# Kernel optimization log

Measured on AMD Instinct MI355X. Metric: run time of the kernel, lower is better.

The kernel has to match this reference:

```python
import jax, jax.numpy as jnp
import numpy as np

N_NODES = 100_000
N_RAND_EDGES = 3_200_000
IN_FEATS, HIDDEN, N_CLASSES = 256, 32, 40


def setup_inputs() -> dict:
    key = jax.random.key(0)
    kf, ks, kd, kw1, kw2 = jax.random.split(key, 5)
    features = jax.random.normal(kf, (N_NODES, IN_FEATS), dtype=jnp.float32)
    # random edges + explicit self loops (mirrors dgl.add_self_loop)
    src = jnp.concatenate([
        jax.random.randint(ks, (N_RAND_EDGES,), 0, N_NODES, dtype=jnp.int32),
        jnp.arange(N_NODES, dtype=jnp.int32),
    ])
    dst = jnp.concatenate([
        jax.random.randint(kd, (N_RAND_EDGES,), 0, N_NODES, dtype=jnp.int32),
        jnp.arange(N_NODES, dtype=jnp.int32),
    ])
    # Glorot-style init as in DGL GraphConv
    W1 = jax.random.normal(kw1, (IN_FEATS, HIDDEN), dtype=jnp.float32) * (2.0 / (IN_FEATS + HIDDEN)) ** 0.5
    b1 = jnp.zeros((HIDDEN,), dtype=jnp.float32)
    W2 = jax.random.normal(kw2, (HIDDEN, N_CLASSES), dtype=jnp.float32) * (2.0 / (HIDDEN + N_CLASSES)) ** 0.5
    b2 = jnp.zeros((N_CLASSES,), dtype=jnp.float32)
    return {"features": features, "src": src, "dst": dst,
            "W1": W1, "b1": b1, "W2": W2, "b2": b2}


def _graph_conv(x, W, b, src, dst, norm_src, norm_dst):
    """DGL GraphConv, norm='both': D_in^{-1/2} A D_out^{-1/2} X W + b.
    Apply W first (cheaper gather when out_feats small); math-identical."""
    h = (x * norm_src[:, None]) @ W              # [N, out]
    msgs = h[src]                                # gather  [E, out]
    agg = jax.ops.segment_sum(msgs, dst, num_segments=N_NODES)  # scatter-add
    return agg * norm_dst[:, None] + b


def reference(features, src, dst, W1, b1, W2, b2):
    ones = jnp.ones(src.shape[0], dtype=jnp.float32)
    out_deg = jax.ops.segment_sum(ones, src, num_segments=N_NODES)
    in_deg = jax.ops.segment_sum(ones, dst, num_segments=N_NODES)
    norm_src = jax.lax.rsqrt(out_deg)            # self loops guarantee deg >= 1
    norm_dst = jax.lax.rsqrt(in_deg)

    x = _graph_conv(features, W1, b1, src, dst, norm_src, norm_dst)
    x = jax.nn.relu(x)
    # F.dropout(training=self.training) is identity at inference
    x = _graph_conv(x, W2, b2, src, dst, norm_src, norm_dst)
    return jax.nn.log_softmax(x, axis=1)
```

## Files before the change

### kernel.cpp

```cpp
#include <hip/hip_runtime.h>
#include <hip/hip_bf16.h>
#include <math.h>

#define BSHIFT 7
#define NBUCK(N) (((N) + 127) >> 7)
#define TILE 8192
#define CAP 5632

typedef short bf16x8 __attribute__((ext_vector_type(8)));
typedef float f32x16 __attribute__((ext_vector_type(16)));

__device__ __forceinline__ unsigned short f2bf(float f) {
    unsigned u = __float_as_uint(f);
    u += 0x7fffu + ((u >> 16) & 1u);
    return (unsigned short)(u >> 16);
}
__device__ __forceinline__ unsigned packbf2(float lo, float hi) {
    return (unsigned)f2bf(lo) | ((unsigned)f2bf(hi) << 16);
}
__device__ __forceinline__ float bf_lo(unsigned u) { return __uint_as_float(u << 16); }
__device__ __forceinline__ float bf_hi(unsigned u) { return __uint_as_float(u & 0xffff0000u); }

__global__ __launch_bounds__(256) void pg_kernel(
    const int* __restrict__ src, const int* __restrict__ dst,
    int* __restrict__ gcurD, int* __restrict__ gcurS,
    int* __restrict__ gbufD, unsigned char* __restrict__ gbufS,
    const float* __restrict__ feat, const float* __restrict__ W1,
    unsigned short* __restrict__ h1, int E, int K, int PB, int N) {
    __shared__ char smem[16896];
    const int t = threadIdx.x;

    if (blockIdx.x < PB) {
        int* cD = (int*)smem;
        int* bD = cD + 800;
        int* cS = bD + 800;
        int* bS = cS + 800;
        const int tile = blockIdx.x * TILE;
        for (int i = t; i < K; i += 256) { cD[i] = 0; cS[i] = 0; }
        __syncthreads();

        int dv[32];
        #pragma unroll
        for (int i = 0; i < 32; ++i) {
            const int e = tile + i * 256 + t;
            dv[i] = (e < E) ? dst[e] : -1;
            if (dv[i] >= 0) {
                atomicAdd(&cD[dv[i] >> BSHIFT], 1);
                atomicAdd(&cS[src[e] >> BSHIFT], 1);
            }
        }
        __syncthreads();
        for (int i = t; i < K; i += 256) {
            int c = cD[i];
            bD[i] = (c ? atomicAdd(&gcurD[i], c) : 0) + i * CAP;
            cD[i] = 0;
            c = cS[i];
            bS[i] = (c ? atomicAdd(&gcurS[i], c) : 0) + i * CAP;
            cS[i] = 0;
        }
        __syncthreads();
        #pragma unroll
        for (int i = 0; i < 32; ++i) {
            if (dv[i] >= 0) {
                const int e = tile + i * 256 + t;
                const int sv = src[e];
                const int b1 = dv[i] >> BSHIFT;
                const int p1 = bD[b1] + atomicAdd(&cD[b1], 1);
                gbufD[p1] = ((dv[i] & 127) << 17) | sv;
                const int b2 = sv >> BSHIFT;
                const int p2 = bS[b2] + atomicAdd(&cS[b2], 1);
                gbufS[p2] = (unsigned char)(sv & 127);
            }
        }
    } else {
        short* W1t = (short*)smem;
        for (int i = t; i < 8192; i += 256) {
            const int k = i >> 5, c = i & 31;
            W1t[c * 264 + k] = (short)f2bf(W1[i]);
        }
        __syncthreads();

        const int l  = t & 63;
        const int wv = t >> 6;
        const int base = (blockIdx.x - PB) * 128 + wv * 32;
        const int m  = l & 31;
        const int kh = (l >> 5) << 3;
        int r = base + m;
        if (r >= N) r = N - 1;
        const float* fr = feat + (size_t)r * 256 + kh;
        const short* wr = &W1t[m * 264 + kh];

        f32x16 acc;
        #pragma unroll
        for (int i = 0; i < 16; ++i) acc[i] = 0.f;

        #pragma unroll
        for (int kb = 0; kb < 16; ++kb) {
            const float4 f0 = *(const float4*)(fr + kb * 16);
            const float4 f1 = *(const float4*)(fr + kb * 16 + 4);
            bf16x8 a;
            a[0] = (short)f2bf(f0.x); a[1] = (short)f2bf(f0.y);
            a[2] = (short)f2bf(f0.z); a[3] = (short)f2bf(f0.w);
            a[4] = (short)f2bf(f1.x); a[5] = (short)f2bf(f1.y);
            a[6] = (short)f2bf(f1.z); a[7] = (short)f2bf(f1.w);
            const bf16x8 b = *(const bf16x8*)(wr + kb * 16);
            acc = __builtin_amdgcn_mfma_f32_32x32x16_bf16(a, b, acc, 0, 0, 0);
        }

        const int rbase = base + ((l >> 5) << 2);
        #pragma unroll
        for (int reg = 0; reg < 16; ++reg) {
            const int row = rbase + (reg & 3) + ((reg >> 2) << 3);
            if (row < N)
                h1[(size_t)row * 32 + m] = f2bf(acc[reg]);
        }
    }
}

__global__ __launch_bounds__(256) void fillS_kernel(
    const int* __restrict__ cntS, const unsigned char* __restrict__ gbufS,
    float* __restrict__ nsrc, int N, int K) {
    __shared__ int cnt[128];
    const int t = threadIdx.x;
    const int b = blockIdx.x;
    if (t < 128) cnt[t] = 0;
    __syncthreads();
    const int bs = b * CAP;
    const int be = bs + min(cntS[b], CAP);
    for (int idx = bs + t; idx < be; idx += 256)
        atomicAdd(&cnt[gbufS[idx]], 1);
    __syncthreads();
    const int n = (b << BSHIFT) + t;
    if (t < 128 && n < N) nsrc[n] = rsqrtf((float)cnt[t]);
}

__global__ __launch_bounds__(512) void fda1_kernel(
    const int* __restrict__ cntD, int* __restrict__ gbufD,
    const unsigned* __restrict__ h1, const float* __restrict__ nsrc,
    const float* __restrict__ b1, int* __restrict__ rowstart,
    int* __restrict__ indeg, float* __restrict__ ndst,
    unsigned* __restrict__ x1s, int N, int K) {
    __shared__ int lraw[CAP];
    __shared__ int lcsr[CAP];
    __shared__ int cnt[128], sc[128], cur[128];
    __shared__ float sb1[32];
    const int t = threadIdx.x;
    const int b = blockIdx.x;
    if (t < 128) cnt[t] = 0;
    if (t >= 128 && t < 160) sb1[t - 128] = b1[t - 128];
    __syncthreads();

    const int bs = b * CAP;
    const int total = min(cntD[b], CAP);
    for (int i = t; i < total; i += 512) {
        const int v = gbufD[bs + i];
        lraw[i] = v;
        atomicAdd(&cnt[v >> 17], 1);
    }
    __syncthreads();
    if (t < 128) sc[t] = cnt[t];
    __syncthreads();
    for (int off = 1; off < 128; off <<= 1) {
        int x = (t < 128 && t >= off) ? sc[t - off] : 0;
        __syncthreads();
        if (t < 128) sc[t] += x;
        __syncthreads();
    }
    if (t < 128) {
        const int deg = cnt[t];
        cur[t] = sc[t] - deg;
        const int n = (b << BSHIFT) + t;
        if (n < N) {
            rowstart[n] = bs + sc[t] - deg;
            indeg[n] = deg;
            ndst[n] = rsqrtf((float)deg);
        }
    }
    __syncthreads();
    for (int i = t; i < total; i += 512) {
        const int v = lraw[i];
        const int pos = atomicAdd(&cur[v >> 17], 1);
        lcsr[pos] = v & 131071;
    }
    __syncthreads();
    for (int i = t; i < total; i += 512) gbufD[bs + i] = lcsr[i];

    const int c  = t & 3;
    const int eg = (t >> 2) & 1;
    const uint4* H = (const uint4*)h1;
    for (int half = 0; half < 2; ++half) {
        const int node = (t >> 3) + half * 64;
        const int n = (b << BSHIFT) + node;
        if (n >= N) continue;
        const int deg = cnt[node];
        const int re = sc[node];
        const int rs = re - deg;
        const int n8 = deg >> 3;
        float a0=0.f,a1=0.f,a2=0.f,a3=0.f,a4=0.f,a5=0.f,a6=0.f,a7=0.f;
        float d0=0.f,d1=0.f,d2=0.f,d3=0.f,d4=0.f,d5=0.f,d6=0.f,d7=0.f;
        for (int i = 0; i < n8; ++i) {
            const int k0 = rs + i * 8 + eg * 4;
            const int s0 = lcsr[k0],     s1 = lcsr[k0 + 1];
            const int s2 = lcsr[k0 + 2], s3 = lcsr[k0 + 3];
            const uint4 q0 = H[(size_t)s0 * 4 + c];
            const uint4 q1 = H[(size_t)s1 * 4 + c];
            const uint4 q2 = H[(size_t)s2 * 4 + c];
            const uint4 q3 = H[(size_t)s3 * 4 + c];
            const float w0 = nsrc[s0], w1 = nsrc[s1];
            const float w2 = nsrc[s2], w3 = nsrc[s3];
            a0 += bf_lo(q0.x)*w0; a1 += bf_hi(q0.x)*w0;
            a2 += bf_lo(q0.y)*w0; a3 += bf_hi(q0.y)*w0;
            a4 += bf_lo(q0.z)*w0; a5 += bf_hi(q0.z)*w0;
            a6 += bf_lo(q0.w)*w0; a7 += bf_hi(q0.w)*w0;
            d0 += bf_lo(q1.x)*w1; d1 += bf_hi(q1.x)*w1;
            d2 += bf_lo(q1.y)*w1; d3 += bf_hi(q1.y)*w1;
            d4 += bf_lo(q1.z)*w1; d5 += bf_hi(q1.z)*w1;
            d6 += bf_lo(q1.w)*w1; d7 += bf_hi(q1.w)*w1;
            a0 += bf_lo(q2.x)*w2; a1 += bf_hi(q2.x)*w2;
            a2 += bf_lo(q2.y)*w2; a3 += bf_hi(q2.y)*w2;
            a4 += bf_lo(q2.z)*w2; a5 += bf_hi(q2.z)*w2;
            a6 += bf_lo(q2.w)*w2; a7 += bf_hi(q2.w)*w2;
            d0 += bf_lo(q3.x)*w3; d1 += bf_hi(q3.x)*w3;
            d2 += bf_lo(q3.y)*w3; d3 += bf_hi(q3.y)*w3;
            d4 += bf_lo(q3.z)*w3; d5 += bf_hi(q3.z)*w3;
            d6 += bf_lo(q3.w)*w3; d7 += bf_hi(q3.w)*w3;
        }
        for (int k = rs + n8 * 8 + eg; k < re; k += 2) {
            const int s0 = lcsr[k];
            const uint4 q0 = H[(size_t)s0 * 4 + c];
            const float w0 = nsrc[s0];
            a0 += bf_lo(q0.x)*w0; a1 += bf_hi(q0.x)*w0;
            a2 += bf_lo(q0.y)*w0; a3 += bf_hi(q0.y)*w0;
            a4 += bf_lo(q0.z)*w0; a5 += bf_hi(q0.z)*w0;
            a6 += bf_lo(q0.w)*w0; a7 += bf_hi(q0.w)*w0;
        }
        a0 += d0; a1 += d1; a2 += d2; a3 += d3;
        a4 += d4; a5 += d5; a6 += d6; a7 += d7;
        a0 += __shfl_xor(a0, 4, 64); a1 += __shfl_xor(a1, 4, 64);
        a2 += __shfl_xor(a2, 4, 64); a3 += __shfl_xor(a3, 4, 64);
        a4 += __shfl_xor(a4, 4, 64); a5 += __shfl_xor(a5, 4, 64);
        a6 += __shfl_xor(a6, 4, 64); a7 += __shfl_xor(a7, 4, 64);
        if (eg == 0) {
            const float nd = rsqrtf((float)deg);
            const float ns = nsrc[n];
            const float* bb = sb1 + c * 8;
            float x0 = fmaxf(a0 * nd + bb[0], 0.f) * ns;
            float x1 = fmaxf(a1 * nd + bb[1], 0.f) * ns;
            float x2 = fmaxf(a2 * nd + bb[2], 0.f) * ns;
            float x3 = fmaxf(a3 * nd + bb[3], 0.f) * ns;
            float x4 = fmaxf(a4 * nd + bb[4], 0.f) * ns;
            float x5 = fmaxf(a5 * nd + bb[5], 0.f) * ns;
            float x6 = fmaxf(a6 * nd + bb[6], 0.f) * ns;
            float x7 = fmaxf(a7 * nd + bb[7], 0.f) * ns;
            uint4 o;
            o.x = packbf2(x0, x1); o.y = packbf2(x2, x3);
            o.z = packbf2(x4, x5); o.w = packbf2(x6, x7);
            ((uint4*)x1s)[(size_t)n * 4 + c] = o;
        }
    }
}

__global__ __launch_bounds__(256) void agg2f_kernel(
    const int* __restrict__ csr_src, const int* __restrict__ rowstart,
    const int* __restrict__ indeg, const unsigned* __restrict__ x1s,
    const float* __restrict__ ndst, const float* __restrict__ W2,
    const float* __restrict__ b2, float* __restrict__ out, int N) {
    __shared__ float sW2[32 * 40];
    __shared__ float sb2[40];
    const int t = threadIdx.x;
    for (int i = t; i < 1280; i += 256) sW2[i] = W2[i];
    if (t < 40) sb2[t] = b2[t];
    __syncthreads();
    const int n = blockIdx.x * 32 + (t >> 3);
    if (n >= N) return;
    const int c  = t & 3;
    const int eg = (t >> 2) & 1;
    const int rs = rowstart[n];
    const int deg = indeg[n];
    const int re = rs + deg;
    const int n8 = deg >> 3;
    float a0=0.f,a1=0.f,a2=0.f,a3=0.f,a4=0.f,a5=0.f,a6=0.f,a7=0.f;
    float d0=0.f,d1=0.f,d2=0.f,d3=0.f,d4=0.f,d5=0.f,d6=0.f,d7=0.f;
    const uint4* H = (const uint4*)x1s;
    for (int i = 0; i < n8; ++i) {
        const int k0 = rs + i * 8 + eg * 4;
        const int s0 = csr_src[k0],     s1 = csr_src[k0 + 1];
        const int s2 = csr_src[k0 + 2], s3 = csr_src[k0 + 3];
        const uint4 q0 = H[(size_t)s0 * 4 + c];
        const uint4 q1 = H[(size_t)s1 * 4 + c];
        const uint4 q2 = H[(size_t)s2 * 4 + c];
        const uint4 q3 = H[(size_t)s3 * 4 + c];
        a0 += bf_lo(q0.x); a1 += bf_hi(q0.x);
        a2 += bf_lo(q0.y); a3 += bf_hi(q0.y);
        a4 += bf_lo(q0.z); a5 += bf_hi(q0.z);
        a6 += bf_lo(q0.w); a7 += bf_hi(q0.w);
        d0 += bf_lo(q1.x); d1 += bf_hi(q1.x);
        d2 += bf_lo(q1.y); d3 += bf_hi(q1.y);
        d4 += bf_lo(q1.z); d5 += bf_hi(q1.z);
        d6 += bf_lo(q1.w); d7 += bf_hi(q1.w);
        a0 += bf_lo(q2.x); a1 += bf_hi(q2.x);
        a2 += bf_lo(q2.y); a3 += bf_hi(q2.y);
        a4 += bf_lo(q2.z); a5 += bf_hi(q2.z);
        a6 += bf_lo(q2.w); a7 += bf_hi(q2.w);
        d0 += bf_lo(q3.x); d1 += bf_hi(q3.x);
        d2 += bf_lo(q3.y); d3 += bf_hi(q3.y);
        d4 += bf_lo(q3.z); d5 += bf_hi(q3.z);
        d6 += bf_lo(q3.w); d7 += bf_hi(q3.w);
    }
    for (int k = rs + n8 * 8 + eg; k < re; k += 2) {
        const int s0 = csr_src[k];
        const uint4 q0 = H[(size_t)s0 * 4 + c];
        a0 += bf_lo(q0.x); a1 += bf_hi(q0.x);
        a2 += bf_lo(q0.y); a3 += bf_hi(q0.y);
        a4 += bf_lo(q0.z); a5 += bf_hi(q0.z);
        a6 += bf_lo(q0.w); a7 += bf_hi(q0.w);
    }
    a0 += d0; a1 += d1; a2 += d2; a3 += d3;
    a4 += d4; a5 += d5; a6 += d6; a7 += d7;
    a0 += __shfl_xor(a0, 4, 64); a1 += __shfl_xor(a1, 4, 64);
    a2 += __shfl_xor(a2, 4, 64); a3 += __shfl_xor(a3, 4, 64);
    a4 += __shfl_xor(a4, 4, 64); a5 += __shfl_xor(a5, 4, 64);
    a6 += __shfl_xor(a6, 4, 64); a7 += __shfl_xor(a7, 4, 64);
    const float nd = ndst[n];
    const float v0 = a0 * nd, v1 = a1 * nd, v2 = a2 * nd, v3 = a3 * nd;
    const float v4 = a4 * nd, v5 = a5 * nd, v6 = a6 * nd, v7 = a7 * nd;

    const int j = t & 7;
    float z[5];
    #pragma unroll
    for (int u = 0; u < 5; ++u) z[u] = sb2[j * 5 + u];
    const int gbase = (t & 63) & ~7;
    #pragma unroll
    for (int cc = 0; cc < 4; ++cc) {
        const int sl = gbase + cc;
        const float w0 = __shfl(v0, sl, 64);
        const float w1 = __shfl(v1, sl, 64);
        const float w2 = __shfl(v2, sl, 64);
        const float w3 = __shfl(v3, sl, 64);
        const float w4 = __shfl(v4, sl, 64);
        const float w5 = __shfl(v5, sl, 64);
        const float w6 = __shfl(v6, sl, 64);
        const float w7 = __shfl(v7, sl, 64);
        const float* Wr = &sW2[(cc * 8) * 40 + j * 5];
        #pragma unroll
        for (int u = 0; u < 5; ++u) {
            z[u] += w0 * Wr[u]       + w1 * Wr[40 + u]  + w2 * Wr[80 + u]  + w3 * Wr[120 + u]
                  + w4 * Wr[160 + u] + w5 * Wr[200 + u] + w6 * Wr[240 + u] + w7 * Wr[280 + u];
        }
    }
    float m = z[0];
    #pragma unroll
    for (int u = 1; u < 5; ++u) m = fmaxf(m, z[u]);
    m = fmaxf(m, __shfl_xor(m, 1, 64));
    m = fmaxf(m, __shfl_xor(m, 2, 64));
    m = fmaxf(m, __shfl_xor(m, 4, 64));
    float s = 0.f;
    #pragma unroll
    for (int u = 0; u < 5; ++u) s += __expf(z[u] - m);
    s += __shfl_xor(s, 1, 64);
    s += __shfl_xor(s, 2, 64);
    s += __shfl_xor(s, 4, 64);
    const float ls = __logf(s);
    float* op = out + (size_t)n * 40 + j * 5;
    #pragma unroll
    for (int u = 0; u < 5; ++u) op[u] = z[u] - m - ls;
}

extern "C" void kernel_launch(void* const* d_in, const int* in_sizes, int n_in,
                              void* d_out, int out_size, void* d_ws, size_t ws_size,
                              hipStream_t stream) {
    const float* feat = (const float*)d_in[0];
    const int*   src  = (const int*)d_in[1];
    const int*   dst  = (const int*)d_in[2];
    const float* W1   = (const float*)d_in[3];
    const float* b1   = (const float*)d_in[4];
    const float* W2   = (const float*)d_in[5];
    const float* b2   = (const float*)d_in[6];
    float* out = (float*)d_out;

    const int N = in_sizes[0] / 256;
    const int E = in_sizes[1];
    const int K = NBUCK(N);

    char* p = (char*)d_ws;
    float* nsrc = (float*)p;                 p += (size_t)N * 4;
    float* ndst = (float*)p;                 p += (size_t)N * 4;
    unsigned* h1  = (unsigned*)p;            p += (size_t)N * 64;
    unsigned* x1s = (unsigned*)p;            p += (size_t)N * 64;
    char* a2dead = (char*)p;                 p += (size_t)N * 128;
    int* rowstart = (int*)p;                 p += (size_t)N * 4;
    int* indeg_i  = (int*)p;                 p += (size_t)N * 4;
    int* gcurD    = (int*)p;                 p += 800 * 4;
    int* gcurS    = (int*)p;                 p += 800 * 4;
    int* gbufD    = (int*)p;                 p += (size_t)K * CAP * 4;
    unsigned char* gbufS = (unsigned char*)a2dead;

    hipMemsetAsync(gcurD, 0, sizeof(int) * 1600, stream);

    const int PB = (E + TILE - 1) / TILE;
    const int GB = (N + 127) / 128;

    pg_kernel<<<PB + GB, 256, 0, stream>>>(src, dst, gcurD, gcurS, gbufD, gbufS,
                                           feat, W1, (unsigned short*)h1, E, K, PB, N);
    fillS_kernel<<<K, 256, 0, stream>>>(gcurS, gbufS, nsrc, N, K);
    fda1_kernel<<<K, 512, 0, stream>>>(gcurD, gbufD, h1, nsrc, b1,
                                       rowstart, indeg_i, ndst, x1s, N, K);
    agg2f_kernel<<<(N + 31) / 32, 256, 0, stream>>>(gbufD, rowstart, indeg_i, x1s, ndst, W2, b2, out, N);
}
```

Baseline: 374.3 us.

## Shard source-degree bucket counters per XCD and prescale h1 by source norm

Result: faster. 342.4 us (-8.5%).

```diff
diff --git a/kernel.cpp b/kernel.cpp
--- a/kernel.cpp
+++ b/kernel.cpp
@@ -6,6 +6,8 @@
 #define NBUCK(N) (((N) + 127) >> 7)
 #define TILE 8192
 #define CAP 5632
+#define CAPS 2040
+#define NXCD 8
 
 typedef short bf16x8 __attribute__((ext_vector_type(8)));
 typedef float f32x16 __attribute__((ext_vector_type(16)));
@@ -20,6 +22,12 @@
 }
 __device__ __forceinline__ float bf_lo(unsigned u) { return __uint_as_float(u << 16); }
 __device__ __forceinline__ float bf_hi(unsigned u) { return __uint_as_float(u & 0xffff0000u); }
+
+__device__ __forceinline__ int xcc_id() {
+    int x;
+    asm volatile("s_getreg_b32 %0, hwreg(HW_REG_XCC_ID)" : "=s"(x));
+    return x & (NXCD - 1);
+}
 
 __global__ __launch_bounds__(256) void pg_kernel(
     const int* __restrict__ src, const int* __restrict__ dst,
@@ -36,6 +44,7 @@
         int* cS = bD + 800;
         int* bS = cS + 800;
         const int tile = blockIdx.x * TILE;
+        const int vx = xcc_id();
         for (int i = t; i < K; i += 256) { cD[i] = 0; cS[i] = 0; }
         __syncthreads();
 
@@ -55,7 +64,7 @@
             bD[i] = (c ? atomicAdd(&gcurD[i], c) : 0) + i * CAP;
             cD[i] = 0;
             c = cS[i];
-            bS[i] = (c ? atomicAdd(&gcurS[i], c) : 0) + i * CAP;
+            bS[i] = (c ? atomicAdd(&gcurS[vx * K + i], c) : 0) + (vx * K + i) * CAPS;
             cS[i] = 0;
         }
         __syncthreads();
@@ -119,19 +128,46 @@
 
 __global__ __launch_bounds__(256) void fillS_kernel(
     const int* __restrict__ cntS, const unsigned char* __restrict__ gbufS,
-    float* __restrict__ nsrc, int N, int K) {
+    float* __restrict__ nsrc, unsigned* __restrict__ h1, int N, int K) {
     __shared__ int cnt[128];
+    __shared__ float sns[128];
     const int t = threadIdx.x;
     const int b = blockIdx.x;
     if (t < 128) cnt[t] = 0;
     __syncthreads();
-    const int bs = b * CAP;
-    const int be = bs + min(cntS[b], CAP);
-    for (int idx = bs + t; idx < be; idx += 256)
-        atomicAdd(&cnt[gbufS[idx]], 1);
-    __syncthreads();
-    const int n = (b << BSHIFT) + t;
-    if (t < 128 && n < N) nsrc[n] = rsqrtf((float)cnt[t]);
+    for (int x = 0; x < NXCD; ++x) {
+        const int seg = x * K + b;
+        const int bs = seg * CAPS;
+        const int be = bs + min(cntS[seg], CAPS);
+        for (int idx = bs + t; idx < be; idx += 256)
+            atomicAdd(&cnt[gbufS[idx]], 1);
+    }
+    __syncthreads();
+    if (t < 128) {
+        const float v = rsqrtf((float)cnt[t]);
+        sns[t] = v;
+        const int n = (b << BSHIFT) + t;
+        if (n < N) nsrc[n] = v;
+    }
+    __syncthreads();
+    const int node = t >> 1;
+    const int n = (b << BSHIFT) + node;
+    if (n < N) {
+        const float ns = sns[node];
+        unsigned* row = h1 + (size_t)n * 16 + (t & 1) * 8;
+        uint4 q0 = *(uint4*)row;
+        uint4 q1 = *(uint4*)(row + 4);
+        q0.x = packbf2(bf_lo(q0.x) * ns, bf_hi(q0.x) * ns);
+        q0.y = packbf2(bf_lo(q0.y) * ns, bf_hi(q0.y) * ns);
+        q0.z = packbf2(bf_lo(q0.z) * ns, bf_hi(q0.z) * ns);
+        q0.w = packbf2(bf_lo(q0.w) * ns, bf_hi(q0.w) * ns);
+        q1.x = packbf2(bf_lo(q1.x) * ns, bf_hi(q1.x) * ns);
+        q1.y = packbf2(bf_lo(q1.y) * ns, bf_hi(q1.y) * ns);
+        q1.z = packbf2(bf_lo(q1.z) * ns, bf_hi(q1.z) * ns);
+        q1.w = packbf2(bf_lo(q1.w) * ns, bf_hi(q1.w) * ns);
+        *(uint4*)row = q0;
+        *(uint4*)(row + 4) = q1;
+    }
 }
 
 __global__ __launch_bounds__(512) void fda1_kernel(
@@ -206,33 +242,30 @@
             const uint4 q1 = H[(size_t)s1 * 4 + c];
             const uint4 q2 = H[(size_t)s2 * 4 + c];
             const uint4 q3 = H[(size_t)s3 * 4 + c];
-            const float w0 = nsrc[s0], w1 = nsrc[s1];
-            const float w2 = nsrc[s2], w3 = nsrc[s3];
-            a0 += bf_lo(q0.x)*w0; a1 += bf_hi(q0.x)*w0;
-            a2 += bf_lo(q0.y)*w0; a3 += bf_hi(q0.y)*w0;
-            a4 += bf_lo(q0.z)*w0; a5 += bf_hi(q0.z)*w0;
-            a6 += bf_lo(q0.w)*w0; a7 += bf_hi(q0.w)*w0;
-            d0 += bf_lo(q1.x)*w1; d1 += bf_hi(q1.x)*w1;
-            d2 += bf_lo(q1.y)*w1; d3 += bf_hi(q1.y)*w1;
-            d4 += bf_lo(q1.z)*w1; d5 += bf_hi(q1.z)*w1;
-            d6 += bf_lo(q1.w)*w1; d7 += bf_hi(q1.w)*w1;
-            a0 += bf_lo(q2.x)*w2; a1 += bf_hi(q2.x)*w2;
-            a2 += bf_lo(q2.y)*w2; a3 += bf_hi(q2.y)*w2;
-            a4 += bf_lo(q2.z)*w2; a5 += bf_hi(q2.z)*w2;
-            a6 += bf_lo(q2.w)*w2; a7 += bf_hi(q2.w)*w2;
-            d0 += bf_lo(q3.x)*w3; d1 += bf_hi(q3.x)*w3;
-            d2 += bf_lo(q3.y)*w3; d3 += bf_hi(q3.y)*w3;
-            d4 += bf_lo(q3.z)*w3; d5 += bf_hi(q3.z)*w3;
-            d6 += bf_lo(q3.w)*w3; d7 += bf_hi(q3.w)*w3;
+            a0 += bf_lo(q0.x); a1 += bf_hi(q0.x);
+            a2 += bf_lo(q0.y); a3 += bf_hi(q0.y);
+            a4 += bf_lo(q0.z); a5 += bf_hi(q0.z);
+            a6 += bf_lo(q0.w); a7 += bf_hi(q0.w);
+            d0 += bf_lo(q1.x); d1 += bf_hi(q1.x);
+            d2 += bf_lo(q1.y); d3 += bf_hi(q1.y);
+            d4 += bf_lo(q1.z); d5 += bf_hi(q1.z);
+            d6 += bf_lo(q1.w); d7 += bf_hi(q1.w);
+            a0 += bf_lo(q2.x); a1 += bf_hi(q2.x);
+            a2 += bf_lo(q2.y); a3 += bf_hi(q2.y);
+            a4 += bf_lo(q2.z); a5 += bf_hi(q2.z);
+            a6 += bf_lo(q2.w); a7 += bf_hi(q2.w);
+            d0 += bf_lo(q3.x); d1 += bf_hi(q3.x);
+            d2 += bf_lo(q3.y); d3 += bf_hi(q3.y);
+            d4 += bf_lo(q3.z); d5 += bf_hi(q3.z);
+            d6 += bf_lo(q3.w); d7 += bf_hi(q3.w);
         }
         for (int k = rs + n8 * 8 + eg; k < re; k += 2) {
             const int s0 = lcsr[k];
             const uint4 q0 = H[(size_t)s0 * 4 + c];
-            const float w0 = nsrc[s0];
-            a0 += bf_lo(q0.x)*w0; a1 += bf_hi(q0.x)*w0;
-            a2 += bf_lo(q0.y)*w0; a3 += bf_hi(q0.y)*w0;
-            a4 += bf_lo(q0.z)*w0; a5 += bf_hi(q0.z)*w0;
-            a6 += bf_lo(q0.w)*w0; a7 += bf_hi(q0.w)*w0;
+            a0 += bf_lo(q0.x); a1 += bf_hi(q0.x);
+            a2 += bf_lo(q0.y); a3 += bf_hi(q0.y);
+            a4 += bf_lo(q0.z); a5 += bf_hi(q0.z);
+            a6 += bf_lo(q0.w); a7 += bf_hi(q0.w);
         }
         a0 += d0; a1 += d1; a2 += d2; a3 += d3;
         a4 += d4; a5 += d5; a6 += d6; a7 += d7;
@@ -391,18 +424,18 @@
     int* rowstart = (int*)p;                 p += (size_t)N * 4;
     int* indeg_i  = (int*)p;                 p += (size_t)N * 4;
     int* gcurD    = (int*)p;                 p += 800 * 4;
-    int* gcurS    = (int*)p;                 p += 800 * 4;
+    int* gcurS    = (int*)p;                 p += (size_t)NXCD * 800 * 4;
     int* gbufD    = (int*)p;                 p += (size_t)K * CAP * 4;
     unsigned char* gbufS = (unsigned char*)a2dead;
 
-    hipMemsetAsync(gcurD, 0, sizeof(int) * 1600, stream);
+    hipMemsetAsync(gcurD, 0, sizeof(int) * (800 + NXCD * 800), stream);
 
     const int PB = (E + TILE - 1) / TILE;
     const int GB = (N + 127) / 128;
 
     pg_kernel<<<PB + GB, 256, 0, stream>>>(src, dst, gcurD, gcurS, gbufD, gbufS,
                                            feat, W1, (unsigned short*)h1, E, K, PB, N);
-    fillS_kernel<<<K, 256, 0, stream>>>(gcurS, gbufS, nsrc, N, K);
+    fillS_kernel<<<K, 256, 0, stream>>>(gcurS, gbufS, nsrc, h1, N, K);
     fda1_kernel<<<K, 512, 0, stream>>>(gcurD, gbufD, h1, nsrc, b1,
                                        rowstart, indeg_i, ndst, x1s, N, K);
     agg2f_kernel<<<(N + 31) / 32, 256, 0, stream>>>(gbufD, rowstart, indeg_i, x1s, ndst, W2, b2, out, N);
```
